# Kernel optimization log

Measured on AMD Instinct MI355X. Metric: run time of the kernel, lower is better.

The kernel has to match this reference:

```python
import math
import jax, jax.numpy as jnp
import numpy as np

B, D, N, KP1 = 64, 128, 500000, 4096  # batch, input_size, output_size, K+1
MOMENTUM = 0.5


def setup_inputs() -> dict:
    key = jax.random.key(0)
    k0, k1, k2, k3, k4, k5 = jax.random.split(key, 6)
    stdv = 1.0 / math.sqrt(D / 3)
    image = jax.random.normal(k0, (B, D), jnp.float32)
    gene = jax.random.normal(k1, (B, D), jnp.float32)
    index = jax.random.randint(k2, (B,), 0, N, dtype=jnp.int32)
    idx = jax.random.randint(k3, (B, KP1), 0, N, dtype=jnp.int32)
    idx = idx.at[:, 0].set(index)  # positive sample in slot 0
    memory_image = jax.random.uniform(k4, (N, D), jnp.float32) * (2 * stdv) - stdv
    memory_gene = jax.random.uniform(k5, (N, D), jnp.float32) * (2 * stdv) - stdv
    return {"image": image, "gene": gene, "memory_image": memory_image,
            "memory_gene": memory_gene, "index": index, "idx": idx}


def _momentum_update(mem, x, index):
    # gather positive rows, momentum blend, L2 normalize, scatter back
    pos = mem[index] * MOMENTUM + x * (1.0 - MOMENTUM)          # [B, D]
    pos = pos / jnp.sqrt(jnp.sum(pos * pos, axis=1, keepdims=True))
    return mem.at[index].set(pos)


def reference(image, gene, memory_image, memory_gene, index, idx):
    # gathered bank rows are detached in the original (weights .detach())
    w_gene = jax.lax.stop_gradient(memory_gene[idx])    # [B, K+1, D]
    w_image = jax.lax.stop_gradient(memory_image[idx])  # [B, K+1, D]
    # bmm([B,K+1,D], [B,D,1]) -> scores [B, K+1]; use_softmax=False branch:
    # stabilized softmax over the K+1 candidates (no temperature division)
    out_image = jax.nn.softmax(jnp.einsum('bkd,bd->bk', w_gene, image), axis=1)
    out_gene = jax.nn.softmax(jnp.einsum('bkd,bd->bk', w_image, gene), axis=1)
    # no_grad momentum scatter-update of the banks
    new_mem_image = _momentum_update(memory_image, jax.lax.stop_gradient(image), index)
    new_mem_gene = _momentum_update(memory_gene, jax.lax.stop_gradient(gene), index)
    return out_image, out_gene, new_mem_image, new_mem_gene
```

## Files before the change

kernel.cpp:

```cpp
#include <hip/hip_runtime.h>
#include <math.h>

constexpr int Bb   = 64;
constexpr int Dd   = 128;
constexpr int KP1  = 4096;
constexpr int Nrow = 500000;
constexpr long NMEM = (long)Nrow * Dd;
constexpr int BK   = Bb * KP1;

constexpr int MSLOT = 16;
constexpr int NGROUP = 31250;
constexpr int GPB    = 15625;
constexpr long WS_NEED = (long)Nrow * 4 * (1 + MSLOT);

typedef float f4 __attribute__((ext_vector_type(4)));

__device__ __forceinline__ float dot8(float4 a, float4 b, float4 x0, float4 x1) {
    return a.x*x0.x + a.y*x0.y + a.z*x0.z + a.w*x0.w
         + b.x*x1.x + b.y*x1.y + b.z*x1.z + b.w*x1.w;
}


__global__ __launch_bounds__(512) void zero_cnt(int* cnt) {
    int i = blockIdx.x * 512 + threadIdx.x;
    for (; i < Nrow; i += gridDim.x * 512) cnt[i] = 0;
}

__global__ __launch_bounds__(512) void build_inv(
    const int* __restrict__ idx, int* __restrict__ cnt, int* __restrict__ entries)
{
    const int j = blockIdx.x * 512 + threadIdx.x;
    const int r = idx[j];
    const int c = atomicAdd(&cnt[r], 1);
    if (c < MSLOT) entries[r * MSLOT + c] = j;
}

__global__ __launch_bounds__(512, 2) void copy_score(
    const float* __restrict__ image, const float* __restrict__ gene,
    const float* __restrict__ mem_image, const float* __restrict__ mem_gene,
    const int* __restrict__ cnt, const int* __restrict__ entries,
    float* __restrict__ out)
{
    const int tid  = threadIdx.x;
    const int half = tid >> 5;
    const int lane = tid & 31;

    __shared__ f4 lxi[2048];
    __shared__ f4 lxg[2048];
    {
        const f4* gi = (const f4*)image;
        const f4* gg = (const f4*)gene;
        #pragma unroll
        for (int u = 0; u < 4; ++u) {
            lxi[u * 512 + tid] = gi[u * 512 + tid];
            lxg[u * 512 + tid] = gg[u * 512 + tid];
        }
    }
    __syncthreads();

    const f4* srcI = (const f4*)mem_image;
    const f4* srcG = (const f4*)mem_gene;
    f4* dst = (f4*)(out + 2 * BK);

    for (int G0 = blockIdx.x * 8; G0 < NGROUP; G0 += gridDim.x * 8) {
        const int gl = (NGROUP - G0 < 8) ? (NGROUP - G0) : 8;
        f4 v[16];
        #pragma unroll
        for (int q = 0; q < 8; ++q) {
            if (q < gl) {
                const int G = G0 + q;
                const f4* s = (G < GPB) ? srcI + (long)G * 1024
                                        : srcG + (long)(G - GPB) * 1024;
                v[2 * q]     = s[tid];
                v[2 * q + 1] = s[512 + tid];
            }
        }
        #pragma unroll
        for (int q = 0; q < 8; ++q) {
            if (q < gl) {
                const int G = G0 + q;
                const long dbase = (long)G * 1024;
                __builtin_nontemporal_store(v[2 * q],     dst + dbase + tid);
                __builtin_nontemporal_store(v[2 * q + 1], dst + dbase + 512 + tid);

                const int bank  = (G < GPB) ? 0 : 1;
                const int rbase = (bank ? (G - GPB) : G) * 32;
                const f4* lx    = bank ? lxi : lxg;
                float* odir     = bank ? out : out + BK;
                #pragma unroll
                for (int s2 = 0; s2 < 2; ++s2) {
                    const int r = rbase + s2 * 16 + half;
                    int n = cnt[r];
                    n = (n < MSLOT) ? n : MSLOT;
                    const f4 rv = v[2 * q + s2];
                    for (int e = 0; e < n; ++e) {
                        const int j = entries[r * MSLOT + e];
                        const f4 xv = lx[(j >> 12) * 32 + lane];
                        float s = rv.x * xv.x + rv.y * xv.y + rv.z * xv.z + rv.w * xv.w;
                        s += __shfl_xor(s, 1);
                        s += __shfl_xor(s, 2);
                        s += __shfl_xor(s, 4);
                        s += __shfl_xor(s, 8);
                        s += __shfl_xor(s, 16);
                        if (lane == 0) odir[j] = s;
                    }
                }
            }
        }
    }
}

__global__ __launch_bounds__(512) void softmax_rows(float* __restrict__ out) {
    const int tid = threadIdx.x;
    f4* row = (f4*)(out + (long)blockIdx.x * KP1);
    __shared__ float red[8];

    f4 a = row[tid], b = row[tid + 512];
    float m = fmaxf(fmaxf(fmaxf(a.x, a.y), fmaxf(a.z, a.w)),
                    fmaxf(fmaxf(b.x, b.y), fmaxf(b.z, b.w)));
    #pragma unroll
    for (int off = 1; off < 64; off <<= 1) m = fmaxf(m, __shfl_xor(m, off));
    if ((tid & 63) == 0) red[tid >> 6] = m;
    __syncthreads();
    if (tid < 64) {
        float tv = (tid < 8) ? red[tid] : -INFINITY;
        #pragma unroll
        for (int off = 1; off < 8; off <<= 1) tv = fmaxf(tv, __shfl_xor(tv, off));
        if (tid == 0) red[0] = tv;
    }
    __syncthreads();
    m = red[0];
    __syncthreads();

    a.x = expf(a.x - m); a.y = expf(a.y - m); a.z = expf(a.z - m); a.w = expf(a.w - m);
    b.x = expf(b.x - m); b.y = expf(b.y - m); b.z = expf(b.z - m); b.w = expf(b.w - m);
    float sum = a.x + a.y + a.z + a.w + b.x + b.y + b.z + b.w;
    #pragma unroll
    for (int off = 1; off < 64; off <<= 1) sum += __shfl_xor(sum, off);
    if ((tid & 63) == 0) red[tid >> 6] = sum;
    __syncthreads();
    if (tid < 64) {
        float tv = (tid < 8) ? red[tid] : 0.f;
        #pragma unroll
        for (int off = 1; off < 8; off <<= 1) tv += __shfl_xor(tv, off);
        if (tid == 0) red[0] = tv;
    }
    __syncthreads();
    const float inv = 1.0f / red[0];
    a *= inv; b *= inv;
    row[tid] = a; row[tid + 512] = b;
}


constexpr long HALF_F4    = NMEM / 4;
constexpr int  CHUNK_F4   = 8192;
constexpr int  FULL_PER_B = 1953;
constexpr long TAIL_BASE  = (long)FULL_PER_B * CHUNK_F4;
constexpr int  CHUNKS_PER_BANK = FULL_PER_B + 1;
constexpr int  NCHUNK     = 2 * CHUNKS_PER_BANK;

__global__ __launch_bounds__(64) void zero_ctr(unsigned* ctr) {
    if (threadIdx.x == 0) *ctr = 0u;
}

__global__ __launch_bounds__(512, 2) void fused_scores_copy(
    const float* __restrict__ image, const float* __restrict__ gene,
    const float* __restrict__ mem_image, const float* __restrict__ mem_gene,
    const int* __restrict__ idx, float* __restrict__ out, unsigned* __restrict__ ctr)
{
    const int tid = threadIdx.x;

    if (blockIdx.x < 128) {
        const int b     = blockIdx.x >> 1;
        const int which = blockIdx.x & 1;
        const float* w = which ? mem_image : mem_gene;
        const float* x = which ? gene : image;
        float* o = out + (long)which * BK + (long)b * KP1;

        __shared__ int   sidx[KP1];
        __shared__ float sv[KP1];
        __shared__ float red[8];

        {
            const int4* s4 = (const int4*)(idx + (long)b * KP1);
            int4* d4 = (int4*)sidx;
            d4[tid]       = s4[tid];
            d4[tid + 512] = s4[tid + 512];
        }
        const int lg  = tid & 15;
        const int grp = tid >> 4;
        float4 x0 = *(const float4*)(x + b * Dd + lg * 8);
        float4 x1 = *(const float4*)(x + b * Dd + lg * 8 + 4);
        __syncthreads();

        for (int j = 0; j < 128; j += 4) {
            const int k0 = grp + (j + 0) * 32;
            const int k1 = grp + (j + 1) * 32;
            const int k2 = grp + (j + 2) * 32;
            const int k3 = grp + (j + 3) * 32;
            const float4* r0 = (const float4*)(w + (long)sidx[k0] * Dd + lg * 8);
            const float4* r1 = (const float4*)(w + (long)sidx[k1] * Dd + lg * 8);
            const float4* r2 = (const float4*)(w + (long)sidx[k2] * Dd + lg * 8);
            const float4* r3 = (const float4*)(w + (long)sidx[k3] * Dd + lg * 8);
            float4 a0 = r0[0], b0 = r0[1];
            float4 a1 = r1[0], b1 = r1[1];
            float4 a2 = r2[0], b2 = r2[1];
            float4 a3 = r3[0], b3 = r3[1];
            float d0 = dot8(a0, b0, x0, x1);
            float d1 = dot8(a1, b1, x0, x1);
            float d2 = dot8(a2, b2, x0, x1);
            float d3 = dot8(a3, b3, x0, x1);
            d0 += __shfl_xor(d0, 1); d1 += __shfl_xor(d1, 1);
            d2 += __shfl_xor(d2, 1); d3 += __shfl_xor(d3, 1);
            d0 += __shfl_xor(d0, 2); d1 += __shfl_xor(d1, 2);
            d2 += __shfl_xor(d2, 2); d3 += __shfl_xor(d3, 2);
            d0 += __shfl_xor(d0, 4); d1 += __shfl_xor(d1, 4);
            d2 += __shfl_xor(d2, 4); d3 += __shfl_xor(d3, 4);
            d0 += __shfl_xor(d0, 8); d1 += __shfl_xor(d1, 8);
            d2 += __shfl_xor(d2, 8); d3 += __shfl_xor(d3, 8);
            if (lg == 0) { sv[k0] = d0; sv[k1] = d1; sv[k2] = d2; sv[k3] = d3; }
        }
        __syncthreads();

        float m = fmaxf(sv[tid], sv[tid + 512]);
        m = fmaxf(m, fmaxf(sv[tid + 1024], sv[tid + 1536]));
        m = fmaxf(m, fmaxf(sv[tid + 2048], sv[tid + 2560]));
        m = fmaxf(m, fmaxf(sv[tid + 3072], sv[tid + 3584]));
        #pragma unroll
        for (int off = 1; off < 64; off <<= 1) m = fmaxf(m, __shfl_xor(m, off));
        if ((tid & 63) == 0) red[tid >> 6] = m;
        __syncthreads();
        if (tid < 64) {
            float tv = (tid < 8) ? red[tid] : -INFINITY;
            #pragma unroll
            for (int off = 1; off < 8; off <<= 1) tv = fmaxf(tv, __shfl_xor(tv, off));
            if (tid == 0) red[0] = tv;
        }
        __syncthreads();
        m = red[0];
        __syncthreads();

        float sum = 0.f;
        #pragma unroll
        for (int r = 0; r < 8; ++r) {
            int k = tid + r * 512;
            float e = expf(sv[k] - m);
            sv[k] = e;
            sum += e;
        }
        #pragma unroll
        for (int off = 1; off < 64; off <<= 1) sum += __shfl_xor(sum, off);
        if ((tid & 63) == 0) red[tid >> 6] = sum;
        __syncthreads();
        if (tid < 64) {
            float tv = (tid < 8) ? red[tid] : 0.f;
            #pragma unroll
            for (int off = 1; off < 8; off <<= 1) tv += __shfl_xor(tv, off);
            if (tid == 0) red[0] = tv;
        }
        __syncthreads();
        const float inv = 1.0f / red[0];
        #pragma unroll
        for (int r = 0; r < 8; ++r) { int k = tid + r * 512; o[k] = sv[k] * inv; }
    }

    const f4* srcI = (const f4*)mem_image;
    const f4* srcG = (const f4*)mem_gene;
    f4* dst = (f4*)(out + 2 * BK);

    __shared__ unsigned sc;
    for (;;) {
        if (tid == 0) sc = atomicAdd(ctr, 1u);
        __syncthreads();
        const unsigned c = sc;
        __syncthreads();
        if (c >= NCHUNK) break;
        const int  bank  = (c < CHUNKS_PER_BANK) ? 0 : 1;
        const int  local = bank ? (int)(c - CHUNKS_PER_BANK) : (int)c;
        const f4*  sbank = bank ? srcG : srcI;
        const long dbank = (long)bank * HALF_F4;
        if (local < FULL_PER_B) {
            const long base = (long)local * CHUNK_F4;
            f4 v[16];
            #pragma unroll
            for (int k = 0; k < 16; ++k) v[k] = sbank[base + k * 512 + tid];
            #pragma unroll
            for (int k = 0; k < 16; ++k)
                __builtin_nontemporal_store(v[k], dst + dbank + base + k * 512 + tid);
        } else {
            f4 v0 = sbank[TAIL_BASE + tid];
            f4 v1 = sbank[TAIL_BASE + 512 + tid];
            __builtin_nontemporal_store(v0, dst + dbank + TAIL_BASE + tid);
            __builtin_nontemporal_store(v1, dst + dbank + TAIL_BASE + 512 + tid);
        }
    }
}

__global__ __launch_bounds__(128) void momentum_update(
    const float* __restrict__ image, const float* __restrict__ gene,
    const float* __restrict__ mem_image, const float* __restrict__ mem_gene,
    const int* __restrict__ index, float* __restrict__ out)
{
    const int b     = blockIdx.x;
    const int which = blockIdx.y;
    const float* mem = which ? mem_gene : mem_image;
    const float* x   = which ? gene : image;
    float* o = out + 2 * BK + (long)which * NMEM;
    const long row = index[b];
    const int d = threadIdx.x;
    float p = mem[row * Dd + d] * 0.5f + x[(long)b * Dd + d] * 0.5f;
    float ss = p * p;
    #pragma unroll
    for (int off = 1; off < 64; off <<= 1) ss += __shfl_xor(ss, off);
    __shared__ float r2[2];
    if ((d & 63) == 0) r2[d >> 6] = ss;
    __syncthreads();
    const float inv = 1.0f / sqrtf(r2[0] + r2[1]);
    o[row * Dd + d] = p * inv;
}

extern "C" void kernel_launch(void* const* d_in, const int* in_sizes, int n_in,
                              void* d_out, int out_size, void* d_ws, size_t ws_size,
                              hipStream_t stream) {
    const float* image     = (const float*)d_in[0];
    const float* gene      = (const float*)d_in[1];
    const float* mem_image = (const float*)d_in[2];
    const float* mem_gene  = (const float*)d_in[3];
    const int*   index     = (const int*)d_in[4];
    const int*   idx       = (const int*)d_in[5];
    float* out = (float*)d_out;

    if ((long)ws_size >= WS_NEED) {
        int* cnt     = (int*)d_ws;
        int* entries = cnt + Nrow;
        zero_cnt<<<dim3(512), 512, 0, stream>>>(cnt);
        build_inv<<<dim3(512), 512, 0, stream>>>(idx, cnt, entries);
        copy_score<<<dim3(2048), 512, 0, stream>>>(
            image, gene, mem_image, mem_gene, cnt, entries, out);
        softmax_rows<<<dim3(128), 512, 0, stream>>>(out);
    } else {
        unsigned* ctr = (unsigned*)d_ws;
        zero_ctr<<<dim3(1), 64, 0, stream>>>(ctr);
        fused_scores_copy<<<dim3(2048), 512, 0, stream>>>(
            image, gene, mem_image, mem_gene, idx, out, ctr);
    }
    momentum_update<<<dim3(64, 2), 128, 0, stream>>>(
        image, gene, mem_image, mem_gene, index, out);
}
```

Before: 261.8 us.

## Stage inverse-index counts in LDS and fuse softmax with momentum update

The copy_score loop now loads each group's per-row counts and first entry into shared memory in one cooperative pass, so the scattered global loads of cnt and entries no longer sit inside the dependent scoring loop. Rows with no entries are skipped early. The separate softmax and momentum-update launches are merged into one epilogue kernel, which removes a launch. Launch grid sizes are also retuned. The trade-off is two __syncthreads per group iteration and extra LDS use.

Measured after the change: 229.1 us. -12.5%, faster.

```diff
diff --git a/kernel.cpp b/kernel.cpp
--- a/kernel.cpp
+++ b/kernel.cpp
@@ -11,6 +11,8 @@
 constexpr int MSLOT = 16;
 constexpr int NGROUP = 31250;
 constexpr int GPB    = 15625;
+constexpr int SGQ    = 8;
+constexpr int NSG    = (NGROUP + SGQ - 1) / SGQ;
 constexpr long WS_NEED = (long)Nrow * 4 * (1 + MSLOT);
 
 typedef float f4 __attribute__((ext_vector_type(4)));
@@ -45,8 +47,10 @@
     const int half = tid >> 5;
     const int lane = tid & 31;
 
-    __shared__ f4 lxi[2048];
-    __shared__ f4 lxg[2048];
+    __shared__ f4  lxi[2048];
+    __shared__ f4  lxg[2048];
+    __shared__ int scnt[256];
+    __shared__ int se0[256];
     {
         const f4* gi = (const f4*)image;
         const f4* gg = (const f4*)gene;
@@ -62,11 +66,12 @@
     const f4* srcG = (const f4*)mem_gene;
     f4* dst = (f4*)(out + 2 * BK);
 
-    for (int G0 = blockIdx.x * 8; G0 < NGROUP; G0 += gridDim.x * 8) {
-        const int gl = (NGROUP - G0 < 8) ? (NGROUP - G0) : 8;
+    for (int G0 = blockIdx.x * SGQ; G0 < NGROUP; G0 += gridDim.x * SGQ) {
+        const int gl = (NGROUP - G0 < SGQ) ? (NGROUP - G0) : SGQ;
+
         f4 v[16];
         #pragma unroll
-        for (int q = 0; q < 8; ++q) {
+        for (int q = 0; q < SGQ; ++q) {
             if (q < gl) {
                 const int G = G0 + q;
                 const f4* s = (G < GPB) ? srcI + (long)G * 1024
@@ -75,80 +80,129 @@
                 v[2 * q + 1] = s[512 + tid];
             }
         }
-        #pragma unroll
-        for (int q = 0; q < 8; ++q) {
+        {
+            const int slot = tid & 255;
+            const int q    = slot >> 5;
             if (q < gl) {
-                const int G = G0 + q;
-                const long dbase = (long)G * 1024;
+                const int G   = G0 + q;
+                const int row = ((G < GPB) ? G : G - GPB) * 32 + (slot & 31);
+                if (tid < 256) scnt[slot] = cnt[row];
+                else           se0[slot]  = entries[row * MSLOT];
+            }
+        }
+
+        #pragma unroll
+        for (int q = 0; q < SGQ; ++q) {
+            if (q < gl) {
+                const long dbase = (long)(G0 + q) * 1024;
                 __builtin_nontemporal_store(v[2 * q],     dst + dbase + tid);
                 __builtin_nontemporal_store(v[2 * q + 1], dst + dbase + 512 + tid);
-
-                const int bank  = (G < GPB) ? 0 : 1;
-                const int rbase = (bank ? (G - GPB) : G) * 32;
+            }
+        }
+        __syncthreads();
+
+        #pragma unroll
+        for (int q = 0; q < SGQ; ++q) {
+            if (q < gl) {
+                const int G     = G0 + q;
+                const int bank  = (G >= GPB);
+                const int rbase = (bank ? G - GPB : G) * 32;
                 const f4* lx    = bank ? lxi : lxg;
                 float* odir     = bank ? out : out + BK;
                 #pragma unroll
                 for (int s2 = 0; s2 < 2; ++s2) {
-                    const int r = rbase + s2 * 16 + half;
-                    int n = cnt[r];
+                    const int slot = q * 32 + s2 * 16 + half;
+                    int n = scnt[slot];
+                    if (n <= 0) continue;
                     n = (n < MSLOT) ? n : MSLOT;
                     const f4 rv = v[2 * q + s2];
-                    for (int e = 0; e < n; ++e) {
-                        const int j = entries[r * MSLOT + e];
+                    int j = se0[slot];
+                    for (int e = 0;;) {
                         const f4 xv = lx[(j >> 12) * 32 + lane];
-                        float s = rv.x * xv.x + rv.y * xv.y + rv.z * xv.z + rv.w * xv.w;
+                        float s = rv.x*xv.x + rv.y*xv.y + rv.z*xv.z + rv.w*xv.w;
                         s += __shfl_xor(s, 1);
                         s += __shfl_xor(s, 2);
                         s += __shfl_xor(s, 4);
                         s += __shfl_xor(s, 8);
                         s += __shfl_xor(s, 16);
                         if (lane == 0) odir[j] = s;
+                        if (++e >= n) break;
+                        j = entries[(rbase + s2 * 16 + half) * MSLOT + e];
                     }
                 }
             }
         }
-    }
-}
-
-__global__ __launch_bounds__(512) void softmax_rows(float* __restrict__ out) {
+        __syncthreads();
+    }
+}
+
+__global__ __launch_bounds__(512) void epilogue(
+    const float* __restrict__ image, const float* __restrict__ gene,
+    const float* __restrict__ mem_image, const float* __restrict__ mem_gene,
+    const int* __restrict__ index, float* __restrict__ out)
+{
     const int tid = threadIdx.x;
-    f4* row = (f4*)(out + (long)blockIdx.x * KP1);
-    __shared__ float red[8];
-
-    f4 a = row[tid], b = row[tid + 512];
-    float m = fmaxf(fmaxf(fmaxf(a.x, a.y), fmaxf(a.z, a.w)),
-                    fmaxf(fmaxf(b.x, b.y), fmaxf(b.z, b.w)));
+
+    if (blockIdx.x < 128) {
+        f4* row = (f4*)(out + (long)blockIdx.x * KP1);
+        __shared__ float red[8];
+
+        f4 a = row[tid], b = row[tid + 512];
+        float m = fmaxf(fmaxf(fmaxf(a.x, a.y), fmaxf(a.z, a.w)),
+                        fmaxf(fmaxf(b.x, b.y), fmaxf(b.z, b.w)));
+        #pragma unroll
+        for (int off = 1; off < 64; off <<= 1) m = fmaxf(m, __shfl_xor(m, off));
+        if ((tid & 63) == 0) red[tid >> 6] = m;
+        __syncthreads();
+        if (tid < 64) {
+            float tv = (tid < 8) ? red[tid] : -INFINITY;
+            #pragma unroll
+            for (int off = 1; off < 8; off <<= 1) tv = fmaxf(tv, __shfl_xor(tv, off));
+            if (tid == 0) red[0] = tv;
+        }
+        __syncthreads();
+        m = red[0];
+        __syncthreads();
+
+        a.x = expf(a.x - m); a.y = expf(a.y - m); a.z = expf(a.z - m); a.w = expf(a.w - m);
+        b.x = expf(b.x - m); b.y = expf(b.y - m); b.z = expf(b.z - m); b.w = expf(b.w - m);
+        float sum = a.x + a.y + a.z + a.w + b.x + b.y + b.z + b.w;
+        #pragma unroll
+        for (int off = 1; off < 64; off <<= 1) sum += __shfl_xor(sum, off);
+        if ((tid & 63) == 0) red[tid >> 6] = sum;
+        __syncthreads();
+        if (tid < 64) {
+            float tv = (tid < 8) ? red[tid] : 0.f;
+            #pragma unroll
+            for (int off = 1; off < 8; off <<= 1) tv += __shfl_xor(tv, off);
+            if (tid == 0) red[0] = tv;
+        }
+        __syncthreads();
+        const float inv = 1.0f / red[0];
+        a *= inv; b *= inv;
+        row[tid] = a; row[tid + 512] = b;
+        return;
+    }
+
+    const int task  = ((blockIdx.x - 128) << 2) | (tid >> 7);
+    const int sub   = tid >> 7;
+    const int d     = tid & 127;
+    const int which = task >> 6;
+    const int b     = task & 63;
+    const float* mem = which ? mem_gene : mem_image;
+    const float* x   = which ? gene : image;
+    float* o = out + 2 * BK + (long)which * NMEM;
+
+    const long row = index[b];
+    float p = mem[row * Dd + d] * 0.5f + x[(long)b * Dd + d] * 0.5f;
+    float ss = p * p;
     #pragma unroll
-    for (int off = 1; off < 64; off <<= 1) m = fmaxf(m, __shfl_xor(m, off));
-    if ((tid & 63) == 0) red[tid >> 6] = m;
+    for (int off = 1; off < 64; off <<= 1) ss += __shfl_xor(ss, off);
+    __shared__ float r2[8];
+    if ((tid & 63) == 0) r2[tid >> 6] = ss;
     __syncthreads();
-    if (tid < 64) {
-        float tv = (tid < 8) ? red[tid] : -INFINITY;
-        #pragma unroll
-        for (int off = 1; off < 8; off <<= 1) tv = fmaxf(tv, __shfl_xor(tv, off));
-        if (tid == 0) red[0] = tv;
-    }
-    __syncthreads();
-    m = red[0];
-    __syncthreads();
-
-    a.x = expf(a.x - m); a.y = expf(a.y - m); a.z = expf(a.z - m); a.w = expf(a.w - m);
-    b.x = expf(b.x - m); b.y = expf(b.y - m); b.z = expf(b.z - m); b.w = expf(b.w - m);
-    float sum = a.x + a.y + a.z + a.w + b.x + b.y + b.z + b.w;
-    #pragma unroll
-    for (int off = 1; off < 64; off <<= 1) sum += __shfl_xor(sum, off);
-    if ((tid & 63) == 0) red[tid >> 6] = sum;
-    __syncthreads();
-    if (tid < 64) {
-        float tv = (tid < 8) ? red[tid] : 0.f;
-        #pragma unroll
-        for (int off = 1; off < 8; off <<= 1) tv += __shfl_xor(tv, off);
-        if (tid == 0) red[0] = tv;
-    }
-    __syncthreads();
-    const float inv = 1.0f / red[0];
-    a *= inv; b *= inv;
-    row[tid] = a; row[tid + 512] = b;
+    const float inv = 1.0f / sqrtf(r2[2 * sub] + r2[2 * sub + 1]);
+    o[row * Dd + d] = p * inv;
 }
 
 
@@ -180,7 +234,6 @@
         __shared__ int   sidx[KP1];
         __shared__ float sv[KP1];
         __shared__ float red[8];
-
         {
             const int4* s4 = (const int4*)(idx + (long)b * KP1);
             int4* d4 = (int4*)sidx;
@@ -333,17 +386,18 @@
     if ((long)ws_size >= WS_NEED) {
         int* cnt     = (int*)d_ws;
         int* entries = cnt + Nrow;
-        zero_cnt<<<dim3(512), 512, 0, stream>>>(cnt);
+        zero_cnt<<<dim3(1024), 512, 0, stream>>>(cnt);
         build_inv<<<dim3(512), 512, 0, stream>>>(idx, cnt, entries);
-        copy_score<<<dim3(2048), 512, 0, stream>>>(
+        copy_score<<<dim3(1954), 512, 0, stream>>>(
             image, gene, mem_image, mem_gene, cnt, entries, out);
-        softmax_rows<<<dim3(128), 512, 0, stream>>>(out);
+        epilogue<<<dim3(160), 512, 0, stream>>>(
+            image, gene, mem_image, mem_gene, index, out);
     } else {
         unsigned* ctr = (unsigned*)d_ws;
         zero_ctr<<<dim3(1), 64, 0, stream>>>(ctr);
         fused_scores_copy<<<dim3(2048), 512, 0, stream>>>(
             image, gene, mem_image, mem_gene, idx, out, ctr);
-    }
-    momentum_update<<<dim3(64, 2), 128, 0, stream>>>(
-        image, gene, mem_image, mem_gene, index, out);
-}
+        momentum_update<<<dim3(64, 2), 128, 0, stream>>>(
+            image, gene, mem_image, mem_gene, index, out);
+    }
+}
```
